# Kernel tuning notes

Hardware: AMD Instinct MI355X
Metric: run time of the kernel (lower is better)

The kernel has to match this reference:

```python
import jax, jax.numpy as jnp
import numpy as np

V, NJ, NCOMP, NBETA = 778, 16, 24, 10
F_CLOSED, N_ANCHOR = 1554, 32
B, NOBJ = 8, 16384
# MANO kinematic tree parents (wrist + 5 fingers x 3 joints)
PARENTS = np.array([-1, 0, 1, 2, 0, 4, 5, 0, 7, 8, 0, 10, 11, 0, 13, 14])


def setup_inputs() -> dict:
    key = jax.random.key(0)
    ks = jax.random.split(key, 12)
    hand_pose = jax.random.normal(ks[0], (B, 3 + 3 + NCOMP), jnp.float32) * 0.1
    obj_points = jax.random.normal(ks[1], (B, NOBJ, 3), jnp.float32) * 0.1
    hand_beta = jax.random.normal(ks[2], (B, NBETA), jnp.float32) * 0.5
    v_template = jax.random.normal(ks[3], (V, 3), jnp.float32) * 0.05
    shapedirs = jax.random.normal(ks[4], (V, 3, NBETA), jnp.float32) * 0.01
    posedirs = jax.random.normal(ks[5], (V, 3, (NJ - 1) * 9), jnp.float32) * 0.01
    J_regressor = jax.nn.softmax(jax.random.normal(ks[6], (NJ, V), jnp.float32), axis=-1)
    lbs_weights = jax.nn.softmax(jax.random.normal(ks[7], (V, NJ), jnp.float32) * 2.0, axis=-1)
    pca_comps = jax.random.normal(ks[8], (NCOMP, (NJ - 1) * 3), jnp.float32) * 0.1
    anchor_weights = jax.nn.softmax(jax.random.normal(ks[9], (N_ANCHOR, 3), jnp.float32), axis=-1)
    closed_faces = jax.random.randint(ks[10], (F_CLOSED, 3), 0, V, jnp.int32)
    anchor_face_idx = jax.random.randint(ks[11], (N_ANCHOR, 3), 0, V, jnp.int32)
    return dict(hand_pose=hand_pose, obj_points=obj_points, hand_beta=hand_beta,
                v_template=v_template, shapedirs=shapedirs, posedirs=posedirs,
                J_regressor=J_regressor, lbs_weights=lbs_weights, pca_comps=pca_comps,
                anchor_weights=anchor_weights, closed_faces=closed_faces,
                anchor_face_idx=anchor_face_idx)


def rodrigues(r):
    # r: [..., 3] axis-angle -> [..., 3, 3] rotation matrix
    theta = jnp.sqrt(jnp.sum(r * r, axis=-1, keepdims=True) + 1e-16)
    k = r / theta
    c = jnp.cos(theta)[..., None]
    s = jnp.sin(theta)[..., None]
    kx, ky, kz = k[..., 0], k[..., 1], k[..., 2]
    zero = jnp.zeros_like(kx)
    K = jnp.stack([zero, -kz, ky, kz, zero, -kx, -ky, kx, zero], axis=-1)
    K = K.reshape(r.shape[:-1] + (3, 3))
    I = jnp.eye(3, dtype=r.dtype)
    return c * I + s * K + (1.0 - c) * k[..., :, None] * k[..., None, :]


def mano_verts(hand_pose, hand_beta, v_template, shapedirs, posedirs,
               J_regressor, lbs_weights, pca_comps):
    b = hand_pose.shape[0]
    trans = hand_pose[:, :3]
    root = hand_pose[:, 3:6]
    hand45 = hand_pose[:, 6:] @ pca_comps  # PCA -> 45-dim pose (flat_hand_mean: no mean add)
    full = jnp.concatenate([root, hand45], axis=-1).reshape(b, NJ, 3)
    R = rodrigues(full)  # [B,16,3,3]
    v_shaped = v_template + jnp.einsum('vdk,bk->bvd', shapedirs, hand_beta)
    J = jnp.einsum('jv,bvd->bjd', J_regressor, v_shaped)  # [B,16,3]
    pose_feat = (R[:, 1:] - jnp.eye(3, dtype=R.dtype)).reshape(b, (NJ - 1) * 9)
    v_posed = v_shaped + jnp.einsum('vdp,bp->bvd', posedirs, pose_feat)

    def make44(Rj, tj):  # [B,3,3],[B,3] -> [B,4,4]
        T = jnp.zeros((b, 4, 4), R.dtype)
        return T.at[:, :3, :3].set(Rj).at[:, :3, 3].set(tj).at[:, 3, 3].set(1.0)

    Ts = [make44(R[:, 0], J[:, 0])]
    for j in range(1, NJ):  # fixed small kinematic chain
        p = int(PARENTS[j])
        Ts.append(jnp.einsum('bmn,bnk->bmk', Ts[p], make44(R[:, j], J[:, j] - J[:, p])))
    T = jnp.stack(Ts, axis=1)  # [B,16,4,4] global joint transforms
    corr = jnp.einsum('bjmn,bjn->bjm', T[..., :3, :3], J)
    A = T.at[..., :3, 3].add(-corr)  # relative-to-rest transforms
    Tw = jnp.einsum('vj,bjmn->bvmn', lbs_weights, A)  # per-vertex skinning transform
    verts = jnp.einsum('bvmn,bvn->bvm', Tw[..., :3, :3], v_posed) + Tw[..., :3, 3]
    return verts + trans[:, None, :]


def vertex_normals(verts, faces):  # verts [B,V,3], faces [F,3]
    def one(v):
        p0, p1, p2 = v[faces[:, 0]], v[faces[:, 1]], v[faces[:, 2]]
        fn = jnp.cross(p1 - p0, p2 - p0)
        vn = (jnp.zeros_like(v).at[faces[:, 0]].add(fn)
              .at[faces[:, 1]].add(fn).at[faces[:, 2]].add(fn))
        return vn / (jnp.linalg.norm(vn, axis=-1, keepdims=True) + 1e-8)
    return jax.vmap(one)(verts)


def reference(hand_pose, obj_points, hand_beta, v_template, shapedirs, posedirs,
              J_regressor, lbs_weights, pca_comps, anchor_weights,
              closed_faces, anchor_face_idx):
    verts = mano_verts(hand_pose, hand_beta, v_template, shapedirs, posedirs,
                       J_regressor, lbs_weights, pca_comps)  # [B,778,3]
    # get_NN: squared cdist obj->hand + argmin (the memory-bound bottleneck)
    d2 = (jnp.sum(obj_points * obj_points, -1, keepdims=True)
          + jnp.sum(verts * verts, -1)[:, None, :]
          - 2.0 * jnp.einsum('bnd,bvd->bnv', obj_points, verts))  # [B,NOBJ,778]
    nn_idx = jnp.argmin(d2, axis=-1)  # [B,NOBJ]
    nn_dist = jnp.take_along_axis(d2, nn_idx[..., None], axis=-1)[..., 0]
    # contact_map_of_m_to_n
    cmap = 1.0 - 2.0 * (jax.nn.sigmoid(100.0 * nn_dist) - 0.5)
    # inter_penetr_loss: interior obj points (behind nearest hand vertex normal)
    normals = vertex_normals(verts, closed_faces)
    nn_vert = jnp.take_along_axis(verts, nn_idx[..., None], axis=1)
    nn_norm = jnp.take_along_axis(normals, nn_idx[..., None], axis=1)
    interior = jnp.sum((nn_vert - obj_points) * nn_norm, axis=-1) > 0.0
    penetration = jnp.sum(jnp.where(interior, nn_dist, 0.0)) / hand_pose.shape[0]
    # AnchorLayer: barycentric anchor points on the hand surface
    contact_candidates = jnp.einsum('ak,bakd->bad', anchor_weights, verts[:, anchor_face_idx])
    return cmap, penetration, verts, contact_candidates
```

## Files before the change

kernel.cpp:

```cpp
#include <hip/hip_runtime.h>
#include <math.h>

#define NV 778
#define NJ 16
#define NCOMP 24
#define NBETA 10
#define FC 1554
#define NA 32
#define NB 8
#define NOBJ 16384
#define VD (NV*3)
#define BCH 584
#define NVQ 832
#define NG 104

__global__ __launch_bounds__(256) void k_blend(
    const float* __restrict__ hp, const float* __restrict__ pca,
    const float* __restrict__ vt, const float* __restrict__ sd,
    const float* __restrict__ pd, const float* __restrict__ beta,
    float* __restrict__ VS, float* __restrict__ VP, float* __restrict__ pen)
{
    int b = blockIdx.x / BCH, c = blockIdx.x % BCH;
    int t = threadIdx.x;
    int wid = t >> 6, lane = t & 63;
    __shared__ float h45[45];
    __shared__ float sR[NJ*9];
    __shared__ float spf[135];

    if (t < 45) {
        float acc = 0.0f;
        #pragma unroll
        for (int k = 0; k < NCOMP; ++k) acc += hp[b*30 + 6 + k] * pca[k*45 + t];
        h45[t] = acc;
    }
    __syncthreads();
    if (t < NJ) {
        float rx, ry, rz;
        if (t == 0) { rx = hp[b*30+3]; ry = hp[b*30+4]; rz = hp[b*30+5]; }
        else        { rx = h45[(t-1)*3]; ry = h45[(t-1)*3+1]; rz = h45[(t-1)*3+2]; }
        float th = sqrtf(rx*rx + ry*ry + rz*rz + 1e-16f);
        float kx = rx/th, ky = ry/th, kz = rz/th;
        float cc = cosf(th), s = sinf(th), o = 1.0f - cc;
        float R[9];
        R[0] = cc + o*kx*kx;     R[1] = -s*kz + o*kx*ky;  R[2] =  s*ky + o*kx*kz;
        R[3] =  s*kz + o*ky*kx;  R[4] = cc + o*ky*ky;     R[5] = -s*kx + o*ky*kz;
        R[6] = -s*ky + o*kz*kx;  R[7] =  s*kx + o*kz*ky;  R[8] = cc + o*kz*kz;
        #pragma unroll
        for (int i = 0; i < 9; ++i) sR[t*9+i] = R[i];
    }
    __syncthreads();
    if (t < 135) {
        int mn = t % 9;
        float d = (mn == 0 || mn == 4 || mn == 8) ? 1.0f : 0.0f;
        spf[t] = sR[9 + t] - d;
    }
    if (b == 0 && c == 0 && t == 0) *pen = 0.0f;
    __syncthreads();

    int r = c*4 + wid;
    if (r < VD) {
        const float* p  = pd + r * 135;
        float accP = p[lane] * spf[lane] + p[lane+64] * spf[lane+64];
        accP += (lane < 7) ? p[lane+128] * spf[lane+128] : 0.0f;

        float accS = (lane < NBETA) ? sd[r*NBETA + lane] * beta[b*NBETA + lane] : 0.0f;

        #pragma unroll
        for (int off = 32; off; off >>= 1) {
            accP += __shfl_down(accP, off, 64);
            accS += __shfl_down(accS, off, 64);
        }
        if (lane == 0) {
            float vs = vt[r] + accS;
            VS[b*VD + r] = vs;
            VP[b*VD + r] = vs + accP;
        }
    }
}

#define PROC1(vk, vidx) {                                                        \
    float d0 = fmaf(-ox0, (vk).x, (vk).w);                                       \
    d0 = fmaf(-oy0, (vk).y, d0); d0 = fmaf(-oz0, (vk).z, d0);                    \
    if (d0 < s0) { s0 = d0; j0 = (vidx); }                                       \
    float d1 = fmaf(-ox1, (vk).x, (vk).w);                                       \
    d1 = fmaf(-oy1, (vk).y, d1); d1 = fmaf(-oz1, (vk).z, d1);                    \
    if (d1 < s1) { s1 = d1; j1 = (vidx); } }

#define PROC8(buf, gbase) {                                                      \
    PROC1((buf)[0], (gbase)+0); PROC1((buf)[1], (gbase)+1);                      \
    PROC1((buf)[2], (gbase)+2); PROC1((buf)[3], (gbase)+3);                      \
    PROC1((buf)[4], (gbase)+4); PROC1((buf)[5], (gbase)+5);                      \
    PROC1((buf)[6], (gbase)+6); PROC1((buf)[7], (gbase)+7); }

__global__ __launch_bounds__(256) void k_mega(
    const float* __restrict__ hp, const float* __restrict__ pca,
    const float* __restrict__ Jreg, const float* __restrict__ VS,
    const float* __restrict__ VP, const float* __restrict__ W,
    const int* __restrict__ faces, const float* __restrict__ aw,
    const int* __restrict__ afi, const float* __restrict__ obj,
    float* __restrict__ verts, float* __restrict__ cmap,
    float* __restrict__ contact, float* __restrict__ pen)
{
    int blk = blockIdx.x;
    int b = blk >> 5;
    int g = blk & 31;
    int t = threadIdx.x, lane = t & 63, wid = t >> 6;

    __shared__ float4 sPK[NVQ];
    __shared__ float sv[VD];
    __shared__ float sn[VD];
    __shared__ float sR[NJ*9];
    __shared__ float sJ[NJ*3];
    __shared__ float4 sA4[NJ*3];
    __shared__ float h45[45];
    __shared__ float wsum[4];

    int n0 = g*512 + t;
    int n1 = n0 + 256;
    const float* o0p = obj + (b*NOBJ + n0)*3;
    const float* o1p = obj + (b*NOBJ + n1)*3;
    float ox0 = o0p[0], oy0 = o0p[1], oz0 = o0p[2];
    float ox1 = o1p[0], oy1 = o1p[1], oz1 = o1p[2];

    if (t < 45) {
        float acc = 0.0f;
        #pragma unroll
        for (int k = 0; k < NCOMP; ++k) acc += hp[b*30 + 6 + k] * pca[k*45 + t];
        h45[t] = acc;
    }
    for (int i = t; i < VD; i += 256) sn[i] = 0.0f;
    if (t < NVQ - NV) sPK[NV + t] = make_float4(0.f, 0.f, 0.f, 1e30f);
    __syncthreads();
    if (t < NJ) {
        float rx, ry, rz;
        if (t == 0) { rx = hp[b*30+3]; ry = hp[b*30+4]; rz = hp[b*30+5]; }
        else        { rx = h45[(t-1)*3]; ry = h45[(t-1)*3+1]; rz = h45[(t-1)*3+2]; }
        float th = sqrtf(rx*rx + ry*ry + rz*rz + 1e-16f);
        float kx = rx/th, ky = ry/th, kz = rz/th;
        float cc = cosf(th), s = sinf(th), o = 1.0f - cc;
        sR[t*9+0] = cc + o*kx*kx;     sR[t*9+1] = -s*kz + o*kx*ky;  sR[t*9+2] =  s*ky + o*kx*kz;
        sR[t*9+3] =  s*kz + o*ky*kx;  sR[t*9+4] = cc + o*ky*ky;     sR[t*9+5] = -s*kx + o*ky*kz;
        sR[t*9+6] = -s*ky + o*kz*kx;  sR[t*9+7] =  s*kx + o*kz*ky;  sR[t*9+8] = cc + o*kz*kz;
    }
    __syncthreads();

    {
        float ac[12];
        #pragma unroll
        for (int q = 0; q < 12; ++q) ac[q] = 0.0f;
        for (int v = lane; v < NV; v += 64) {
            const float* p = VS + b*VD + v*3;
            float x = p[0], y = p[1], z = p[2];
            #pragma unroll
            for (int jj = 0; jj < 4; ++jj) {
                float w = Jreg[(4*wid + jj)*NV + v];
                ac[jj*3+0] += w*x; ac[jj*3+1] += w*y; ac[jj*3+2] += w*z;
            }
        }
        #pragma unroll
        for (int q = 0; q < 12; ++q)
            for (int off = 32; off; off >>= 1) ac[q] += __shfl_down(ac[q], off, 64);
        if (lane == 0) {
            #pragma unroll
            for (int q = 0; q < 12; ++q) sJ[(4*wid + q/3)*3 + (q%3)] = ac[q];
        }
    }
    __syncthreads();

    if (t < 3) {
        const int par[NJ] = {-1,0,1,2,0,4,5,0,7,8,0,10,11,0,13,14};
        int m = t;
        float Tr[NJ][3], Tt[NJ];
        Tr[0][0] = sR[m*3+0]; Tr[0][1] = sR[m*3+1]; Tr[0][2] = sR[m*3+2];
        Tt[0] = sJ[m];
        #pragma unroll
        for (int j = 1; j < NJ; ++j) {
            int p = par[j];
            float t0 = sJ[j*3+0] - sJ[p*3+0];
            float t1 = sJ[j*3+1] - sJ[p*3+1];
            float t2 = sJ[j*3+2] - sJ[p*3+2];
            float a0 = Tr[p][0], a1 = Tr[p][1], a2 = Tr[p][2];
            #pragma unroll
            for (int n = 0; n < 3; ++n)
                Tr[j][n] = a0*sR[j*9+n] + a1*sR[j*9+3+n] + a2*sR[j*9+6+n];
            Tt[j] = a0*t0 + a1*t1 + a2*t2 + Tt[p];
        }
        #pragma unroll
        for (int j = 0; j < NJ; ++j) {
            float corr = Tr[j][0]*sJ[j*3] + Tr[j][1]*sJ[j*3+1] + Tr[j][2]*sJ[j*3+2];
            sA4[j*3 + m] = make_float4(Tr[j][0], Tr[j][1], Tr[j][2], Tt[j] - corr);
        }
    }
    __syncthreads();

    float tx = hp[b*30+0], ty = hp[b*30+1], tz = hp[b*30+2];
    for (int v = t; v < NV; v += 256) {
        float4 r0 = make_float4(0,0,0,0), r1 = make_float4(0,0,0,0), r2 = make_float4(0,0,0,0);
        const float* w = W + v * NJ;
        for (int j = 0; j < NJ; ++j) {
            float wj = w[j];
            float4 A0 = sA4[j*3+0], A1 = sA4[j*3+1], A2 = sA4[j*3+2];
            r0.x += wj*A0.x; r0.y += wj*A0.y; r0.z += wj*A0.z; r0.w += wj*A0.w;
            r1.x += wj*A1.x; r1.y += wj*A1.y; r1.z += wj*A1.z; r1.w += wj*A1.w;
            r2.x += wj*A2.x; r2.y += wj*A2.y; r2.z += wj*A2.z; r2.w += wj*A2.w;
        }
        float px = VP[b*VD + v*3], py = VP[b*VD + v*3+1], pz = VP[b*VD + v*3+2];
        float x = r0.x*px + r0.y*py + r0.z*pz + r0.w + tx;
        float y = r1.x*px + r1.y*py + r1.z*pz + r1.w + ty;
        float z = r2.x*px + r2.y*py + r2.z*pz + r2.w + tz;
        sv[v*3] = x; sv[v*3+1] = y; sv[v*3+2] = z;
        sPK[v] = make_float4(x, y, z, 0.5f*(x*x + y*y + z*z));
        if (g == 0) {
            int i = b*NV + v;
            verts[i*3] = x; verts[i*3+1] = y; verts[i*3+2] = z;
        }
    }
    __syncthreads();

    for (int f = t; f < FC; f += 256) {
        int i0 = faces[f*3], i1 = faces[f*3+1], i2 = faces[f*3+2];
        float ax = sv[i1*3+0]-sv[i0*3+0], ay = sv[i1*3+1]-sv[i0*3+1], az = sv[i1*3+2]-sv[i0*3+2];
        float bx = sv[i2*3+0]-sv[i0*3+0], by = sv[i2*3+1]-sv[i0*3+1], bz = sv[i2*3+2]-sv[i0*3+2];
        float cx = ay*bz - az*by, cy = az*bx - ax*bz, cz = ax*by - ay*bx;
        atomicAdd(&sn[i0*3+0], cx); atomicAdd(&sn[i0*3+1], cy); atomicAdd(&sn[i0*3+2], cz);
        atomicAdd(&sn[i1*3+0], cx); atomicAdd(&sn[i1*3+1], cy); atomicAdd(&sn[i1*3+2], cz);
        atomicAdd(&sn[i2*3+0], cx); atomicAdd(&sn[i2*3+1], cy); atomicAdd(&sn[i2*3+2], cz);
    }
    __syncthreads();

    if (g == 0 && t < NA*3) {
        int a = t / 3, d = t % 3;
        float acc = 0.0f;
        #pragma unroll
        for (int k = 0; k < 3; ++k)
            acc += aw[a*3 + k] * sv[afi[a*3 + k]*3 + d];
        contact[b*NA*3 + t] = acc;
    }

    float s0 = 1e30f, s1 = 1e30f;
    int j0 = 0, j1 = 0;
    {
        float4 A[8], B[8];
        #pragma unroll
        for (int k = 0; k < 8; ++k) A[k] = sPK[k];
        for (int gg = 0; gg + 2 <= NG; gg += 2) {
            #pragma unroll
            for (int k = 0; k < 8; ++k) B[k] = sPK[(gg+1)*8 + k];
            PROC8(A, gg*8);
            if (gg + 2 < NG) {
                #pragma unroll
                for (int k = 0; k < 8; ++k) A[k] = sPK[(gg+2)*8 + k];
            }
            PROC8(B, (gg+1)*8);
        }
    }

    float osq0 = ox0*ox0 + oy0*oy0 + oz0*oz0;
    float d20 = 2.0f * s0 + osq0;
    cmap[b*NOBJ + n0] = 2.0f / (1.0f + __expf(100.0f * d20));
    float4 q0 = sPK[j0];
    float dp0 = (q0.x - ox0)*sn[j0*3+0] + (q0.y - oy0)*sn[j0*3+1] + (q0.z - oz0)*sn[j0*3+2];
    float p = (dp0 > 0.0f) ? d20 : 0.0f;

    float osq1 = ox1*ox1 + oy1*oy1 + oz1*oz1;
    float d21 = 2.0f * s1 + osq1;
    cmap[b*NOBJ + n1] = 2.0f / (1.0f + __expf(100.0f * d21));
    float4 q1 = sPK[j1];
    float dp1 = (q1.x - ox1)*sn[j1*3+0] + (q1.y - oy1)*sn[j1*3+1] + (q1.z - oz1)*sn[j1*3+2];
    p += (dp1 > 0.0f) ? d21 : 0.0f;

    for (int off = 32; off; off >>= 1) p += __shfl_down(p, off, 64);
    if (lane == 0) wsum[wid] = p;
    __syncthreads();
    if (t == 0) atomicAdd(pen, (wsum[0] + wsum[1] + wsum[2] + wsum[3]) * (1.0f / NB));
}

extern "C" void kernel_launch(void* const* d_in, const int* in_sizes, int n_in,
                              void* d_out, int out_size, void* d_ws, size_t ws_size,
                              hipStream_t stream)
{
    const float* hp    = (const float*)d_in[0];
    const float* obj   = (const float*)d_in[1];
    const float* beta  = (const float*)d_in[2];
    const float* vt    = (const float*)d_in[3];
    const float* sd    = (const float*)d_in[4];
    const float* pd    = (const float*)d_in[5];
    const float* Jreg  = (const float*)d_in[6];
    const float* W     = (const float*)d_in[7];
    const float* pca   = (const float*)d_in[8];
    const float* aw    = (const float*)d_in[9];
    const int*   faces = (const int*)d_in[10];
    const int*   afi   = (const int*)d_in[11];

    float* out     = (float*)d_out;
    float* cmap    = out;
    float* pen     = out + NB*NOBJ;
    float* verts   = out + NB*NOBJ + 1;
    float* contact = out + NB*NOBJ + 1 + NB*NV*3;

    float* ws   = (float*)d_ws;
    float* VS   = ws;
    float* VP   = VS + NB*VD;

    k_blend<<<NB*BCH, 256, 0, stream>>>(hp, pca, vt, sd, pd, beta, VS, VP, pen);
    k_mega <<<NB*32, 256, 0, stream>>>(hp, pca, Jreg, VS, VP, W, faces, aw, afi,
                                       obj, verts, cmap, contact, pen);
}
```

Before: 144.2 us.

## Split skinning into per-batch kernel and precompute joint regression linearly in beta

```diff
diff --git a/kernel.cpp b/kernel.cpp
--- a/kernel.cpp
+++ b/kernel.cpp
@@ -13,15 +13,38 @@
 #define BCH 584
 #define NVQ 832
 #define NG 104
+#define NCB 3
 
 __global__ __launch_bounds__(256) void k_blend(
     const float* __restrict__ hp, const float* __restrict__ pca,
     const float* __restrict__ vt, const float* __restrict__ sd,
     const float* __restrict__ pd, const float* __restrict__ beta,
-    float* __restrict__ VS, float* __restrict__ VP, float* __restrict__ pen)
+    const float* __restrict__ Jreg,
+    float* __restrict__ VP, float* __restrict__ C0, float* __restrict__ C1,
+    float* __restrict__ pen)
 {
-    int b = blockIdx.x / BCH, c = blockIdx.x % BCH;
+    int bid = blockIdx.x;
     int t = threadIdx.x;
+
+    if (bid >= NB*BCH) {
+        int gid = (bid - NB*BCH)*256 + t;
+        if (gid < 528) {
+            int jd, k;
+            if (gid < 48) { jd = gid; k = -1; }
+            else          { jd = (gid-48)/NBETA; k = (gid-48)%NBETA; }
+            int j = jd/3, d = jd%3;
+            const float* jr = Jreg + j*NV;
+            float acc = 0.0f;
+            for (int v = 0; v < NV; ++v) {
+                float x = (k < 0) ? vt[v*3+d] : sd[(v*3+d)*NBETA + k];
+                acc += jr[v] * x;
+            }
+            if (k < 0) C0[jd] = acc; else C1[jd*NBETA + k] = acc;
+        }
+        return;
+    }
+
+    int b = bid / BCH, c = bid % BCH;
     int wid = t >> 6, lane = t & 63;
     __shared__ float h45[45];
     __shared__ float sR[NJ*9];
@@ -54,7 +77,7 @@
         float d = (mn == 0 || mn == 4 || mn == 8) ? 1.0f : 0.0f;
         spf[t] = sR[9 + t] - d;
     }
-    if (b == 0 && c == 0 && t == 0) *pen = 0.0f;
+    if (bid == 0 && t == 0) *pen = 0.0f;
     __syncthreads();
 
     int r = c*4 + wid;
@@ -70,57 +93,27 @@
             accP += __shfl_down(accP, off, 64);
             accS += __shfl_down(accS, off, 64);
         }
-        if (lane == 0) {
-            float vs = vt[r] + accS;
-            VS[b*VD + r] = vs;
-            VP[b*VD + r] = vs + accP;
-        }
+        if (lane == 0) VP[b*VD + r] = vt[r] + accS + accP;
     }
 }
 
-#define PROC1(vk, vidx) {                                                        \
-    float d0 = fmaf(-ox0, (vk).x, (vk).w);                                       \
-    d0 = fmaf(-oy0, (vk).y, d0); d0 = fmaf(-oz0, (vk).z, d0);                    \
-    if (d0 < s0) { s0 = d0; j0 = (vidx); }                                       \
-    float d1 = fmaf(-ox1, (vk).x, (vk).w);                                       \
-    d1 = fmaf(-oy1, (vk).y, d1); d1 = fmaf(-oz1, (vk).z, d1);                    \
-    if (d1 < s1) { s1 = d1; j1 = (vidx); } }
-
-#define PROC8(buf, gbase) {                                                      \
-    PROC1((buf)[0], (gbase)+0); PROC1((buf)[1], (gbase)+1);                      \
-    PROC1((buf)[2], (gbase)+2); PROC1((buf)[3], (gbase)+3);                      \
-    PROC1((buf)[4], (gbase)+4); PROC1((buf)[5], (gbase)+5);                      \
-    PROC1((buf)[6], (gbase)+6); PROC1((buf)[7], (gbase)+7); }
-
-__global__ __launch_bounds__(256) void k_mega(
+__global__ __launch_bounds__(256) void k_skel2(
     const float* __restrict__ hp, const float* __restrict__ pca,
-    const float* __restrict__ Jreg, const float* __restrict__ VS,
-    const float* __restrict__ VP, const float* __restrict__ W,
+    const float* __restrict__ beta,
+    const float* __restrict__ C0, const float* __restrict__ C1,
+    const float* __restrict__ W, const float* __restrict__ VP,
     const int* __restrict__ faces, const float* __restrict__ aw,
-    const int* __restrict__ afi, const float* __restrict__ obj,
-    float* __restrict__ verts, float* __restrict__ cmap,
-    float* __restrict__ contact, float* __restrict__ pen)
+    const int* __restrict__ afi,
+    float* __restrict__ verts, float4* __restrict__ PK,
+    float* __restrict__ NRM, float* __restrict__ contact)
 {
-    int blk = blockIdx.x;
-    int b = blk >> 5;
-    int g = blk & 31;
-    int t = threadIdx.x, lane = t & 63, wid = t >> 6;
-
-    __shared__ float4 sPK[NVQ];
-    __shared__ float sv[VD];
-    __shared__ float sn[VD];
+    int b = blockIdx.x, t = threadIdx.x;
+    __shared__ float h45[45];
     __shared__ float sR[NJ*9];
     __shared__ float sJ[NJ*3];
     __shared__ float4 sA4[NJ*3];
-    __shared__ float h45[45];
-    __shared__ float wsum[4];
-
-    int n0 = g*512 + t;
-    int n1 = n0 + 256;
-    const float* o0p = obj + (b*NOBJ + n0)*3;
-    const float* o1p = obj + (b*NOBJ + n1)*3;
-    float ox0 = o0p[0], oy0 = o0p[1], oz0 = o0p[2];
-    float ox1 = o1p[0], oy1 = o1p[1], oz1 = o1p[2];
+    __shared__ float sv[VD];
+    __shared__ float sn[VD];
 
     if (t < 45) {
         float acc = 0.0f;
@@ -129,8 +122,9 @@
         h45[t] = acc;
     }
     for (int i = t; i < VD; i += 256) sn[i] = 0.0f;
-    if (t < NVQ - NV) sPK[NV + t] = make_float4(0.f, 0.f, 0.f, 1e30f);
-    __syncthreads();
+    if (t < NVQ - NV) PK[b*NVQ + NV + t] = make_float4(0.f, 0.f, 0.f, 1e30f);
+    __syncthreads();
+
     if (t < NJ) {
         float rx, ry, rz;
         if (t == 0) { rx = hp[b*30+3]; ry = hp[b*30+4]; rz = hp[b*30+5]; }
@@ -142,28 +136,12 @@
         sR[t*9+3] =  s*kz + o*ky*kx;  sR[t*9+4] = cc + o*ky*ky;     sR[t*9+5] = -s*kx + o*ky*kz;
         sR[t*9+6] = -s*ky + o*kz*kx;  sR[t*9+7] =  s*kx + o*kz*ky;  sR[t*9+8] = cc + o*kz*kz;
     }
-    __syncthreads();
-
-    {
-        float ac[12];
-        #pragma unroll
-        for (int q = 0; q < 12; ++q) ac[q] = 0.0f;
-        for (int v = lane; v < NV; v += 64) {
-            const float* p = VS + b*VD + v*3;
-            float x = p[0], y = p[1], z = p[2];
-            #pragma unroll
-            for (int jj = 0; jj < 4; ++jj) {
-                float w = Jreg[(4*wid + jj)*NV + v];
-                ac[jj*3+0] += w*x; ac[jj*3+1] += w*y; ac[jj*3+2] += w*z;
-            }
-        }
-        #pragma unroll
-        for (int q = 0; q < 12; ++q)
-            for (int off = 32; off; off >>= 1) ac[q] += __shfl_down(ac[q], off, 64);
-        if (lane == 0) {
-            #pragma unroll
-            for (int q = 0; q < 12; ++q) sJ[(4*wid + q/3)*3 + (q%3)] = ac[q];
-        }
+    if (t >= 64 && t < 64 + NJ*3) {
+        int o = t - 64;
+        float acc = C0[o];
+        #pragma unroll
+        for (int k = 0; k < NBETA; ++k) acc += C1[o*NBETA + k] * beta[b*NBETA + k];
+        sJ[o] = acc;
     }
     __syncthreads();
 
@@ -209,11 +187,9 @@
         float y = r1.x*px + r1.y*py + r1.z*pz + r1.w + ty;
         float z = r2.x*px + r2.y*py + r2.z*pz + r2.w + tz;
         sv[v*3] = x; sv[v*3+1] = y; sv[v*3+2] = z;
-        sPK[v] = make_float4(x, y, z, 0.5f*(x*x + y*y + z*z));
-        if (g == 0) {
-            int i = b*NV + v;
-            verts[i*3] = x; verts[i*3+1] = y; verts[i*3+2] = z;
-        }
+        int i = b*NV + v;
+        verts[i*3] = x; verts[i*3+1] = y; verts[i*3+2] = z;
+        PK[b*NVQ + v] = make_float4(x, y, z, 0.5f*(x*x + y*y + z*z));
     }
     __syncthreads();
 
@@ -228,7 +204,8 @@
     }
     __syncthreads();
 
-    if (g == 0 && t < NA*3) {
+    for (int i = t; i < VD; i += 256) NRM[b*VD + i] = sn[i];
+    if (t < NA*3) {
         int a = t / 3, d = t % 3;
         float acc = 0.0f;
         #pragma unroll
@@ -236,6 +213,45 @@
             acc += aw[a*3 + k] * sv[afi[a*3 + k]*3 + d];
         contact[b*NA*3 + t] = acc;
     }
+}
+
+#define PROC1(vk, vidx) {                                                        \
+    float d0 = fmaf(-ox0, (vk).x, (vk).w);                                       \
+    d0 = fmaf(-oy0, (vk).y, d0); d0 = fmaf(-oz0, (vk).z, d0);                    \
+    if (d0 < s0) { s0 = d0; j0 = (vidx); }                                       \
+    float d1 = fmaf(-ox1, (vk).x, (vk).w);                                       \
+    d1 = fmaf(-oy1, (vk).y, d1); d1 = fmaf(-oz1, (vk).z, d1);                    \
+    if (d1 < s1) { s1 = d1; j1 = (vidx); } }
+
+#define PROC8(buf, gbase) {                                                      \
+    PROC1((buf)[0], (gbase)+0); PROC1((buf)[1], (gbase)+1);                      \
+    PROC1((buf)[2], (gbase)+2); PROC1((buf)[3], (gbase)+3);                      \
+    PROC1((buf)[4], (gbase)+4); PROC1((buf)[5], (gbase)+5);                      \
+    PROC1((buf)[6], (gbase)+6); PROC1((buf)[7], (gbase)+7); }
+
+__global__ __launch_bounds__(256) void k_nn(const float* __restrict__ obj,
+                                            const float4* __restrict__ PK,
+                                            const float* __restrict__ NRM,
+                                            float* __restrict__ cmap,
+                                            float* __restrict__ pen)
+{
+    int blk = blockIdx.x;
+    int b = blk >> 5;
+    int g = blk & 31;
+    int t = threadIdx.x, lane = t & 63, wid = t >> 6;
+
+    __shared__ float4 sPK[NVQ];
+    __shared__ float wsum[4];
+
+    int n0 = g*512 + t;
+    int n1 = n0 + 256;
+    const float* o0p = obj + (b*NOBJ + n0)*3;
+    const float* o1p = obj + (b*NOBJ + n1)*3;
+    float ox0 = o0p[0], oy0 = o0p[1], oz0 = o0p[2];
+    float ox1 = o1p[0], oy1 = o1p[1], oz1 = o1p[2];
+
+    for (int i = t; i < NVQ; i += 256) sPK[i] = PK[b*NVQ + i];
+    __syncthreads();
 
     float s0 = 1e30f, s1 = 1e30f;
     int j0 = 0, j1 = 0;
@@ -255,18 +271,21 @@
         }
     }
 
+    int base = b * NV;
     float osq0 = ox0*ox0 + oy0*oy0 + oz0*oz0;
     float d20 = 2.0f * s0 + osq0;
     cmap[b*NOBJ + n0] = 2.0f / (1.0f + __expf(100.0f * d20));
     float4 q0 = sPK[j0];
-    float dp0 = (q0.x - ox0)*sn[j0*3+0] + (q0.y - oy0)*sn[j0*3+1] + (q0.z - oz0)*sn[j0*3+2];
+    float dp0 = (q0.x - ox0)*NRM[(base+j0)*3+0] + (q0.y - oy0)*NRM[(base+j0)*3+1]
+              + (q0.z - oz0)*NRM[(base+j0)*3+2];
     float p = (dp0 > 0.0f) ? d20 : 0.0f;
 
     float osq1 = ox1*ox1 + oy1*oy1 + oz1*oz1;
     float d21 = 2.0f * s1 + osq1;
     cmap[b*NOBJ + n1] = 2.0f / (1.0f + __expf(100.0f * d21));
     float4 q1 = sPK[j1];
-    float dp1 = (q1.x - ox1)*sn[j1*3+0] + (q1.y - oy1)*sn[j1*3+1] + (q1.z - oz1)*sn[j1*3+2];
+    float dp1 = (q1.x - ox1)*NRM[(base+j1)*3+0] + (q1.y - oy1)*NRM[(base+j1)*3+1]
+              + (q1.z - oz1)*NRM[(base+j1)*3+2];
     p += (dp1 > 0.0f) ? d21 : 0.0f;
 
     for (int off = 32; off; off >>= 1) p += __shfl_down(p, off, 64);
@@ -299,10 +318,15 @@
     float* contact = out + NB*NOBJ + 1 + NB*NV*3;
 
     float* ws   = (float*)d_ws;
-    float* VS   = ws;
-    float* VP   = VS + NB*VD;
-
-    k_blend<<<NB*BCH, 256, 0, stream>>>(hp, pca, vt, sd, pd, beta, VS, VP, pen);
-    k_mega <<<NB*32, 256, 0, stream>>>(hp, pca, Jreg, VS, VP, W, faces, aw, afi,
-                                       obj, verts, cmap, contact, pen);
+    float4* PK  = (float4*)ws;
+    float* NRM  = ws + NB*NVQ*4;
+    float* VP   = NRM + NB*VD;
+    float* C0   = VP + NB*VD;
+    float* C1   = C0 + 48;
+
+    k_blend<<<NB*BCH + NCB, 256, 0, stream>>>(hp, pca, vt, sd, pd, beta, Jreg,
+                                              VP, C0, C1, pen);
+    k_skel2<<<NB, 256, 0, stream>>>(hp, pca, beta, C0, C1, W, VP, faces, aw, afi,
+                                    verts, PK, NRM, contact);
+    k_nn   <<<NB*32, 256, 0, stream>>>(obj, PK, NRM, cmap, pen);
 }
```

New measurement: 266.6 us. +84.9%, slower.
